# Kernel tuning notes

Measured on AMD Instinct MI355X. Metric: run time of the kernel, lower is better.

Reference implementation:

```python
import jax, jax.numpy as jnp
import numpy as np

B, C, H, W = 4, 64, 64, 64


def setup_inputs() -> dict:
    key = jax.random.key(0)
    k1, k2, k3, k4, k5 = jax.random.split(key, 5)
    return {
        "x": jax.random.normal(k1, (B, C, H, W), dtype=jnp.float32),
        "w_qkv": jax.random.normal(k2, (3 * C, C), dtype=jnp.float32) * (1.0 / np.sqrt(C)),
        "b_qkv": jax.random.normal(k3, (3 * C,), dtype=jnp.float32) * 0.02,
        "w_proj": jax.random.normal(k4, (C, C), dtype=jnp.float32) * (1.0 / np.sqrt(C)),
        "b_proj": jax.random.normal(k5, (C,), dtype=jnp.float32) * 0.02,
    }


def reference(x, w_qkv, b_qkv, w_proj, b_proj):
    b, c, h, w = x.shape
    xf = x.reshape(b, c, h * w)                                  # [B, C, N]
    # 1x1 Conv1d == per-position linear over channels
    qkv = jnp.einsum('oc,bcn->bon', w_qkv, xf) + b_qkv[None, :, None]  # [B, 3C, N]
    q, k, v = jnp.split(qkv, 3, axis=1)                          # each [B, C, N]
    scores = jnp.einsum('bcn,bcm->bnm', q, k) / (c ** 0.5)       # [B, N, N]
    attn = jax.nn.softmax(scores, axis=-1)
    out = jnp.einsum('bcm,bnm->bcn', v, attn)                    # [B, C, N]
    out = jnp.einsum('oc,bcn->bon', w_proj, out) + b_proj[None, :, None]
    return out.reshape(b, c, h, w) + x
```

## Files before the change

### kernel.cpp

```cpp
#include <hip/hip_runtime.h>

typedef __bf16 bf16x8 __attribute__((ext_vector_type(8)));
typedef float f32x4 __attribute__((ext_vector_type(4)));

#define NB 4
#define NC 64
#define NN 4096
#define SPLIT 8

#define QSCALE (0.125f * 1.44269504088896340736f)

__global__ __launch_bounds__(256) void qkv_kernel(
    const float* __restrict__ x, const float* __restrict__ wqkv,
    const float* __restrict__ bqkv,
    __bf16* __restrict__ Qg, __bf16* __restrict__ Kg, __bf16* __restrict__ Vg)
{
  const int b = blockIdx.y;
  const int z = blockIdx.z;
  const int tsel = z >> 2;
  const int obase = (z & 3) * 16;
  const int n = blockIdx.x * 256 + threadIdx.x;
  const float wscale = (tsel == 0) ? QSCALE : 1.0f;

  __shared__ float wsh[16 * 64];
  __shared__ float bsh[16];
#pragma unroll
  for (int k = 0; k < 4; k++)
    wsh[threadIdx.x + k * 256] =
        wqkv[(tsel * 64 + obase) * 64 + threadIdx.x + k * 256] * wscale;
  if (threadIdx.x < 16)
    bsh[threadIdx.x] = bqkv[tsel * 64 + obase + threadIdx.x] * wscale;
  __syncthreads();

  float xv[64];
#pragma unroll
  for (int c = 0; c < 64; c++)
    xv[c] = x[((size_t)(b * 64 + c)) * NN + n];

  float a[16];
#pragma unroll
  for (int j = 0; j < 16; j++) a[j] = bsh[j];
#pragma unroll
  for (int c4 = 0; c4 < 64; c4 += 4) {
#pragma unroll
    for (int j = 0; j < 16; j++) {
      const float4 wv = *(const float4*)&wsh[j * 64 + c4];
      a[j] = fmaf(wv.x, xv[c4 + 0], a[j]);
      a[j] = fmaf(wv.y, xv[c4 + 1], a[j]);
      a[j] = fmaf(wv.z, xv[c4 + 2], a[j]);
      a[j] = fmaf(wv.w, xv[c4 + 3], a[j]);
    }
  }

  if (tsel == 2) {
#pragma unroll
    for (int j = 0; j < 16; j++)
      Vg[((size_t)(b * 64 + obase + j)) * NN + n] = (__bf16)a[j];
  } else {
    __bf16* base = (tsel == 0 ? Qg : Kg);
#pragma unroll
    for (int g = 0; g < 2; g++) {
      bf16x8 pk;
#pragma unroll
      for (int j = 0; j < 8; j++) pk[j] = (__bf16)a[g * 8 + j];
      *(bf16x8*)(base + ((size_t)(b * NN + n)) * 64 + obase + g * 8) = pk;
    }
  }
}

__global__ __launch_bounds__(256) void flash_kernel(
    const __bf16* __restrict__ Q, const __bf16* __restrict__ K,
    const __bf16* __restrict__ V, __bf16* __restrict__ Opart,
    float* __restrict__ lpart)
{
  const int b = blockIdx.y;
  const int s = blockIdx.z;
  const int tid = threadIdx.x;
  const int wave = tid >> 6;
  const int lane = tid & 63;
  const int quad = lane >> 4;
  const int l16 = lane & 15;

  __shared__ __bf16 Kt[64 * 72];
  __shared__ __bf16 Vt[64 * 72];
  __shared__ __bf16 Pt[4][32 * 72];

  const int q0 = blockIdx.x * 128 + wave * 32;

  bf16x8 qf[2][2];
#pragma unroll
  for (int qt = 0; qt < 2; qt++) {
    const __bf16* qrow = Q + ((size_t)(b * NN + q0 + qt * 16 + l16)) * 64;
    qf[qt][0] = *(const bf16x8*)(qrow + quad * 8);
    qf[qt][1] = *(const bf16x8*)(qrow + 32 + quad * 8);
  }

  f32x4 acc[2][4];
#pragma unroll
  for (int qt = 0; qt < 2; qt++)
#pragma unroll
    for (int ct = 0; ct < 4; ct++) acc[qt][ct] = (f32x4){0.f, 0.f, 0.f, 0.f};
  float l[2][4];
#pragma unroll
  for (int qt = 0; qt < 2; qt++)
#pragma unroll
    for (int r = 0; r < 4; r++) l[qt][r] = 0.f;

  const int kbeg = s * (NN / SPLIT);
  const int kend = kbeg + (NN / SPLIT);
  for (int kt0 = kbeg; kt0 < kend; kt0 += 64) {
    __syncthreads();
#pragma unroll
    for (int it = 0; it < 2; it++) {
      const int chunk = tid + it * 256;
      const int row = chunk >> 3, col8 = (chunk & 7) * 8;
      *(bf16x8*)(&Kt[row * 72 + col8]) =
          *(const bf16x8*)(K + ((size_t)(b * NN + kt0 + row)) * 64 + col8);
      *(bf16x8*)(&Vt[row * 72 + col8]) =
          *(const bf16x8*)(V + ((size_t)(b * 64 + row)) * NN + kt0 + col8);
    }
    __syncthreads();

#pragma unroll
    for (int t = 0; t < 4; t++) {
      const bf16x8 kf0 = *(const bf16x8*)(&Kt[(t * 16 + l16) * 72 + quad * 8]);
      const bf16x8 kf1 = *(const bf16x8*)(&Kt[(t * 16 + l16) * 72 + 32 + quad * 8]);
#pragma unroll
      for (int qt = 0; qt < 2; qt++) {
        f32x4 z = (f32x4){0.f, 0.f, 0.f, 0.f};
        z = __builtin_amdgcn_mfma_f32_16x16x32_bf16(qf[qt][0], kf0, z, 0, 0, 0);
        z = __builtin_amdgcn_mfma_f32_16x16x32_bf16(qf[qt][1], kf1, z, 0, 0, 0);
#pragma unroll
        for (int r = 0; r < 4; r++) {
          const float p = exp2f(z[r]);
          l[qt][r] += p;
          Pt[wave][(qt * 16 + quad * 4 + r) * 72 + t * 16 + l16] = (__bf16)p;
        }
      }
    }

#pragma unroll
    for (int kb = 0; kb < 2; kb++) {
      const bf16x8 pf0 = *(const bf16x8*)(&Pt[wave][l16 * 72 + kb * 32 + quad * 8]);
      const bf16x8 pf1 = *(const bf16x8*)(&Pt[wave][(16 + l16) * 72 + kb * 32 + quad * 8]);
#pragma unroll
      for (int ct = 0; ct < 4; ct++) {
        const bf16x8 vf = *(const bf16x8*)(&Vt[(ct * 16 + l16) * 72 + kb * 32 + quad * 8]);
        acc[0][ct] = __builtin_amdgcn_mfma_f32_16x16x32_bf16(pf0, vf, acc[0][ct], 0, 0, 0);
        acc[1][ct] = __builtin_amdgcn_mfma_f32_16x16x32_bf16(pf1, vf, acc[1][ct], 0, 0, 0);
      }
    }
  }

#pragma unroll
  for (int qt = 0; qt < 2; qt++) {
#pragma unroll
    for (int r = 0; r < 4; r++) {
      float lr = l[qt][r];
      lr += __shfl_xor(lr, 1);
      lr += __shfl_xor(lr, 2);
      lr += __shfl_xor(lr, 4);
      lr += __shfl_xor(lr, 8);
      l[qt][r] = lr;
    }
    const int qb = q0 + qt * 16;
#pragma unroll
    for (int ct = 0; ct < 4; ct++)
#pragma unroll
      for (int r = 0; r < 4; r++)
        Opart[(((size_t)((s * NB + b)) * NN) + qb + quad * 4 + r) * 64 + ct * 16 + l16] =
            (__bf16)acc[qt][ct][r];
    if (l16 == 0) {
#pragma unroll
      for (int r = 0; r < 4; r++)
        lpart[((size_t)(s * NB + b)) * NN + qb + quad * 4 + r] = l[qt][r];
    }
  }
}

__global__ __launch_bounds__(256) void combine_proj_kernel(
    const __bf16* __restrict__ Opart, const float* __restrict__ lpart,
    const float* __restrict__ wproj, const float* __restrict__ bproj,
    const float* __restrict__ x, float* __restrict__ out)
{
  const int b = blockIdx.y;
  const int n0 = blockIdx.x * 32;
  const int tid = threadIdx.x;

  __shared__ float Ot[64 * 36];
  __shared__ float wT[64 * 66];
  __shared__ float lsh[32];
  __shared__ float bsh[64];

  if (tid < 32) {
    float lt = 0.f;
#pragma unroll
    for (int s = 0; s < SPLIT; s++)
      lt += lpart[((size_t)(s * NB + b)) * NN + n0 + tid];
    lsh[tid] = 1.0f / lt;
  }
  if (tid < 64) bsh[tid] = bproj[tid];
#pragma unroll
  for (int k = 0; k < 16; k++) {
    const int i = tid + k * 256;
    wT[(i & 63) * 66 + (i >> 6)] = wproj[i];
  }
  __syncthreads();

  {
    const int row = tid >> 3;
    const int col8 = (tid & 7) * 8;
    float o[8];
#pragma unroll
    for (int j = 0; j < 8; j++) o[j] = 0.f;
#pragma unroll
    for (int s = 0; s < SPLIT; s++) {
      const bf16x8 v = *(const bf16x8*)(
          Opart + (((size_t)(s * NB + b)) * NN + n0 + row) * 64 + col8);
#pragma unroll
      for (int j = 0; j < 8; j++) o[j] += (float)v[j];
    }
    const float rin = lsh[row];
#pragma unroll
    for (int j = 0; j < 8; j++) Ot[(col8 + j) * 36 + row] = o[j] * rin;
  }
  __syncthreads();

  const int co = (tid >> 3) * 2;
  const int ng = (tid & 7) * 4;
  float a0[4], a1[4];
#pragma unroll
  for (int j = 0; j < 4; j++) { a0[j] = bsh[co]; a1[j] = bsh[co + 1]; }
  for (int cin = 0; cin < 64; cin++) {
    const float4 ov = *(const float4*)&Ot[cin * 36 + ng];
    const float2 wv = *(const float2*)&wT[cin * 66 + co];
    a0[0] = fmaf(wv.x, ov.x, a0[0]); a0[1] = fmaf(wv.x, ov.y, a0[1]);
    a0[2] = fmaf(wv.x, ov.z, a0[2]); a0[3] = fmaf(wv.x, ov.w, a0[3]);
    a1[0] = fmaf(wv.y, ov.x, a1[0]); a1[1] = fmaf(wv.y, ov.y, a1[1]);
    a1[2] = fmaf(wv.y, ov.z, a1[2]); a1[3] = fmaf(wv.y, ov.w, a1[3]);
  }

#pragma unroll
  for (int i = 0; i < 2; i++) {
    float* ai = (i == 0) ? a0 : a1;
    const size_t base = ((size_t)(b * 64 + co + i)) * NN + n0 + ng;
    const float4 xr = *(const float4*)&x[base];
    float4 r;
    r.x = ai[0] + xr.x; r.y = ai[1] + xr.y;
    r.z = ai[2] + xr.z; r.w = ai[3] + xr.w;
    *(float4*)&out[base] = r;
  }
}

extern "C" void kernel_launch(void* const* d_in, const int* in_sizes, int n_in,
                              void* d_out, int out_size, void* d_ws, size_t ws_size,
                              hipStream_t stream) {
  const float* x     = (const float*)d_in[0];
  const float* wqkv  = (const float*)d_in[1];
  const float* bqkv  = (const float*)d_in[2];
  const float* wproj = (const float*)d_in[3];
  const float* bproj = (const float*)d_in[4];
  float* out = (float*)d_out;

  char* ws = (char*)d_ws;
  __bf16* Q     = (__bf16*)(ws);
  __bf16* K     = (__bf16*)(ws + (2u << 20));
  __bf16* V     = (__bf16*)(ws + (4u << 20));
  __bf16* Opart = (__bf16*)(ws + (6u << 20));
  float*  lpart = (float*)(ws + (23u << 20));

  qkv_kernel<<<dim3(16, NB, 12), 256, 0, stream>>>(x, wqkv, bqkv, Q, K, V);
  flash_kernel<<<dim3(32, NB, SPLIT), 256, 0, stream>>>(Q, K, V, Opart, lpart);
  combine_proj_kernel<<<dim3(128, NB), 256, 0, stream>>>(Opart, lpart, wproj,
                                                         bproj, x, out);
}
```

Measured before the change: 117.8 us.

## Transpose MFMA operands in flash kernel and retile QKV projection per thread

The flash kernel swaps MFMA A/B operands so each lane holds four consecutive key scores for one query. That lets P be written as packed bf16x4, replaces the per-row 16-lane shuffle reductions with two shuffles, and stores Opart channel-major. The combine kernel reads the new Opart layout with contiguous loads along n. The QKV kernel now computes 8 output channels for 2 positions per thread, using float2 loads and packed stores. This trades register usage and a different LDS write pattern for fewer shuffles and wider memory ops.

New measurement: 117.3 us. Within noise of the previous version (-0.4%).

```diff
diff --git a/kernel.cpp b/kernel.cpp
--- a/kernel.cpp
+++ b/kernel.cpp
@@ -1,6 +1,8 @@
 #include <hip/hip_runtime.h>
 
 typedef __bf16 bf16x8 __attribute__((ext_vector_type(8)));
+typedef __bf16 bf16x4 __attribute__((ext_vector_type(4)));
+typedef __bf16 bf16x2 __attribute__((ext_vector_type(2)));
 typedef float f32x4 __attribute__((ext_vector_type(4)));
 
 #define NB 4
@@ -15,56 +17,61 @@
     const float* __restrict__ bqkv,
     __bf16* __restrict__ Qg, __bf16* __restrict__ Kg, __bf16* __restrict__ Vg)
 {
+  const int tid = threadIdx.x;
   const int b = blockIdx.y;
   const int z = blockIdx.z;
-  const int tsel = z >> 2;
-  const int obase = (z & 3) * 16;
-  const int n = blockIdx.x * 256 + threadIdx.x;
+  const int tsel = z >> 3;
+  const int obase = (z & 7) * 8;
+  const int n = blockIdx.x * 512 + tid * 2;
   const float wscale = (tsel == 0) ? QSCALE : 1.0f;
 
-  __shared__ float wsh[16 * 64];
-  __shared__ float bsh[16];
-#pragma unroll
-  for (int k = 0; k < 4; k++)
-    wsh[threadIdx.x + k * 256] =
-        wqkv[(tsel * 64 + obase) * 64 + threadIdx.x + k * 256] * wscale;
-  if (threadIdx.x < 16)
-    bsh[threadIdx.x] = bqkv[tsel * 64 + obase + threadIdx.x] * wscale;
+  __shared__ float wsh[8 * 64];
+  __shared__ float bsh[8];
+  wsh[tid]       = wqkv[(tsel * 64 + obase) * 64 + tid] * wscale;
+  wsh[tid + 256] = wqkv[(tsel * 64 + obase) * 64 + tid + 256] * wscale;
+  if (tid < 8) bsh[tid] = bqkv[tsel * 64 + obase + tid] * wscale;
   __syncthreads();
 
-  float xv[64];
-#pragma unroll
-  for (int c = 0; c < 64; c++)
-    xv[c] = x[((size_t)(b * 64 + c)) * NN + n];
-
-  float a[16];
-#pragma unroll
-  for (int j = 0; j < 16; j++) a[j] = bsh[j];
+  float xa[64], xb[64];
+#pragma unroll
+  for (int c = 0; c < 64; c++) {
+    const float2 t = *(const float2*)&x[((size_t)(b * 64 + c)) * NN + n];
+    xa[c] = t.x; xb[c] = t.y;
+  }
+
+  float aa[8], ab[8];
+#pragma unroll
+  for (int j = 0; j < 8; j++) { aa[j] = bsh[j]; ab[j] = bsh[j]; }
 #pragma unroll
   for (int c4 = 0; c4 < 64; c4 += 4) {
 #pragma unroll
-    for (int j = 0; j < 16; j++) {
+    for (int j = 0; j < 8; j++) {
       const float4 wv = *(const float4*)&wsh[j * 64 + c4];
-      a[j] = fmaf(wv.x, xv[c4 + 0], a[j]);
-      a[j] = fmaf(wv.y, xv[c4 + 1], a[j]);
-      a[j] = fmaf(wv.z, xv[c4 + 2], a[j]);
-      a[j] = fmaf(wv.w, xv[c4 + 3], a[j]);
+      aa[j] = fmaf(wv.x, xa[c4 + 0], aa[j]);
+      aa[j] = fmaf(wv.y, xa[c4 + 1], aa[j]);
+      aa[j] = fmaf(wv.z, xa[c4 + 2], aa[j]);
+      aa[j] = fmaf(wv.w, xa[c4 + 3], aa[j]);
+      ab[j] = fmaf(wv.x, xb[c4 + 0], ab[j]);
+      ab[j] = fmaf(wv.y, xb[c4 + 1], ab[j]);
+      ab[j] = fmaf(wv.z, xb[c4 + 2], ab[j]);
+      ab[j] = fmaf(wv.w, xb[c4 + 3], ab[j]);
     }
   }
 
   if (tsel == 2) {
 #pragma unroll
-    for (int j = 0; j < 16; j++)
-      Vg[((size_t)(b * 64 + obase + j)) * NN + n] = (__bf16)a[j];
+    for (int j = 0; j < 8; j++) {
+      bf16x2 pv;
+      pv[0] = (__bf16)aa[j]; pv[1] = (__bf16)ab[j];
+      *(bf16x2*)(Vg + ((size_t)(b * 64 + obase + j)) * NN + n) = pv;
+    }
   } else {
     __bf16* base = (tsel == 0 ? Qg : Kg);
-#pragma unroll
-    for (int g = 0; g < 2; g++) {
-      bf16x8 pk;
-#pragma unroll
-      for (int j = 0; j < 8; j++) pk[j] = (__bf16)a[g * 8 + j];
-      *(bf16x8*)(base + ((size_t)(b * NN + n)) * 64 + obase + g * 8) = pk;
-    }
+    bf16x8 p0, p1;
+#pragma unroll
+    for (int j = 0; j < 8; j++) { p0[j] = (__bf16)aa[j]; p1[j] = (__bf16)ab[j]; }
+    *(bf16x8*)(base + ((size_t)(b * NN + n)) * 64 + obase) = p0;
+    *(bf16x8*)(base + ((size_t)(b * NN + n + 1)) * 64 + obase) = p1;
   }
 }
 
@@ -100,11 +107,7 @@
   for (int qt = 0; qt < 2; qt++)
 #pragma unroll
     for (int ct = 0; ct < 4; ct++) acc[qt][ct] = (f32x4){0.f, 0.f, 0.f, 0.f};
-  float l[2][4];
-#pragma unroll
-  for (int qt = 0; qt < 2; qt++)
-#pragma unroll
-    for (int r = 0; r < 4; r++) l[qt][r] = 0.f;
+  float l[2] = {0.f, 0.f};
 
   const int kbeg = s * (NN / SPLIT);
   const int kend = kbeg + (NN / SPLIT);
@@ -128,14 +131,15 @@
 #pragma unroll
       for (int qt = 0; qt < 2; qt++) {
         f32x4 z = (f32x4){0.f, 0.f, 0.f, 0.f};
-        z = __builtin_amdgcn_mfma_f32_16x16x32_bf16(qf[qt][0], kf0, z, 0, 0, 0);
-        z = __builtin_amdgcn_mfma_f32_16x16x32_bf16(qf[qt][1], kf1, z, 0, 0, 0);
-#pragma unroll
-        for (int r = 0; r < 4; r++) {
-          const float p = exp2f(z[r]);
-          l[qt][r] += p;
-          Pt[wave][(qt * 16 + quad * 4 + r) * 72 + t * 16 + l16] = (__bf16)p;
-        }
+        z = __builtin_amdgcn_mfma_f32_16x16x32_bf16(kf0, qf[qt][0], z, 0, 0, 0);
+        z = __builtin_amdgcn_mfma_f32_16x16x32_bf16(kf1, qf[qt][1], z, 0, 0, 0);
+        const float p0 = exp2f(z[0]), p1 = exp2f(z[1]);
+        const float p2 = exp2f(z[2]), p3 = exp2f(z[3]);
+        l[qt] += (p0 + p1) + (p2 + p3);
+        bf16x4 pk;
+        pk[0] = (__bf16)p0; pk[1] = (__bf16)p1;
+        pk[2] = (__bf16)p2; pk[3] = (__bf16)p3;
+        *(bf16x4*)(&Pt[wave][(qt * 16 + l16) * 72 + t * 16 + quad * 4]) = pk;
       }
     }
 
@@ -146,35 +150,25 @@
 #pragma unroll
       for (int ct = 0; ct < 4; ct++) {
         const bf16x8 vf = *(const bf16x8*)(&Vt[(ct * 16 + l16) * 72 + kb * 32 + quad * 8]);
-        acc[0][ct] = __builtin_amdgcn_mfma_f32_16x16x32_bf16(pf0, vf, acc[0][ct], 0, 0, 0);
-        acc[1][ct] = __builtin_amdgcn_mfma_f32_16x16x32_bf16(pf1, vf, acc[1][ct], 0, 0, 0);
+        acc[0][ct] = __builtin_amdgcn_mfma_f32_16x16x32_bf16(vf, pf0, acc[0][ct], 0, 0, 0);
+        acc[1][ct] = __builtin_amdgcn_mfma_f32_16x16x32_bf16(vf, pf1, acc[1][ct], 0, 0, 0);
       }
     }
   }
 
 #pragma unroll
   for (int qt = 0; qt < 2; qt++) {
-#pragma unroll
-    for (int r = 0; r < 4; r++) {
-      float lr = l[qt][r];
-      lr += __shfl_xor(lr, 1);
-      lr += __shfl_xor(lr, 2);
-      lr += __shfl_xor(lr, 4);
-      lr += __shfl_xor(lr, 8);
-      l[qt][r] = lr;
-    }
-    const int qb = q0 + qt * 16;
+    float lr = l[qt];
+    lr += __shfl_xor(lr, 16);
+    lr += __shfl_xor(lr, 32);
+    if (quad == 0)
+      lpart[((size_t)(s * NB + b)) * NN + q0 + qt * 16 + l16] = lr;
 #pragma unroll
     for (int ct = 0; ct < 4; ct++)
 #pragma unroll
       for (int r = 0; r < 4; r++)
-        Opart[(((size_t)((s * NB + b)) * NN) + qb + quad * 4 + r) * 64 + ct * 16 + l16] =
-            (__bf16)acc[qt][ct][r];
-    if (l16 == 0) {
-#pragma unroll
-      for (int r = 0; r < 4; r++)
-        lpart[((size_t)(s * NB + b)) * NN + qb + quad * 4 + r] = l[qt][r];
-    }
+        Opart[(((size_t)(s * NB + b)) * 64 + ct * 16 + quad * 4 + r) * NN +
+              q0 + qt * 16 + l16] = (__bf16)acc[qt][ct][r];
   }
 }
 
@@ -208,21 +202,20 @@
   __syncthreads();
 
   {
-    const int row = tid >> 3;
-    const int col8 = (tid & 7) * 8;
+    const int c = tid >> 2;
+    const int n8 = (tid & 3) * 8;
     float o[8];
 #pragma unroll
     for (int j = 0; j < 8; j++) o[j] = 0.f;
 #pragma unroll
     for (int s = 0; s < SPLIT; s++) {
       const bf16x8 v = *(const bf16x8*)(
-          Opart + (((size_t)(s * NB + b)) * NN + n0 + row) * 64 + col8);
+          Opart + (((size_t)(s * NB + b)) * 64 + c) * NN + n0 + n8);
 #pragma unroll
       for (int j = 0; j < 8; j++) o[j] += (float)v[j];
     }
-    const float rin = lsh[row];
-#pragma unroll
-    for (int j = 0; j < 8; j++) Ot[(col8 + j) * 36 + row] = o[j] * rin;
+#pragma unroll
+    for (int j = 0; j < 8; j++) Ot[c * 36 + n8 + j] = o[j] * lsh[n8 + j];
   }
   __syncthreads();
 
@@ -269,7 +262,7 @@
   __bf16* Opart = (__bf16*)(ws + (6u << 20));
   float*  lpart = (float*)(ws + (23u << 20));
 
-  qkv_kernel<<<dim3(16, NB, 12), 256, 0, stream>>>(x, wqkv, bqkv, Q, K, V);
+  qkv_kernel<<<dim3(8, NB, 24), 256, 0, stream>>>(x, wqkv, bqkv, Q, K, V);
   flash_kernel<<<dim3(32, NB, SPLIT), 256, 0, stream>>>(Q, K, V, Opart, lpart);
   combine_proj_kernel<<<dim3(128, NB), 256, 0, stream>>>(Opart, lpart, wproj,
                                                          bproj, x, out);
```
